# Performance work log

Measured on AMD Instinct MI355X. Metric: run time of the kernel, lower is better.

## Reference

```python
import jax, jax.numpy as jnp
import numpy as np

BS, T, N, M, P = 1024, 128, 128, 256, 256


def _lstm_cell(xin, h, c, Wih, Whh, bih, bhh):
    # PyTorch LSTMCell: gates ordered i, f, g, o
    z = xin @ Wih.T + bih + h @ Whh.T + bhh
    i, f, g, o = jnp.split(z, 4, axis=1)
    i = jax.nn.sigmoid(i); f = jax.nn.sigmoid(f)
    g = jnp.tanh(g); o = jax.nn.sigmoid(o)
    c2 = f * c + i * g
    return o * jnp.tanh(c2), c2


def setup_inputs() -> dict:
    key = jax.random.key(0)
    ks = jax.random.split(key, 24)
    s = 0.05
    return {
        "x": jax.random.normal(ks[0], (BS, T, N), jnp.float32),
        "y_known": jax.random.normal(ks[1], (BS, T, 1), jnp.float32),
        "We": jax.random.normal(ks[2], (T, 2 * M), jnp.float32) * s,
        "Ue": jax.random.normal(ks[3], (T, T), jnp.float32) * s,
        "Ve": jax.random.normal(ks[4], (1, T), jnp.float32) * s,
        "Wih_e": jax.random.normal(ks[5], (4 * M, N), jnp.float32) * s,
        "Whh_e": jax.random.normal(ks[6], (4 * M, M), jnp.float32) * s,
        "bih_e": jax.random.normal(ks[7], (4 * M,), jnp.float32) * s,
        "bhh_e": jax.random.normal(ks[8], (4 * M,), jnp.float32) * s,
        "Wd": jax.random.normal(ks[9], (M, 2 * P), jnp.float32) * s,
        "Ud": jax.random.normal(ks[10], (M, M), jnp.float32) * s,
        "Vd": jax.random.normal(ks[11], (1, M), jnp.float32) * s,
        "Wih_d": jax.random.normal(ks[12], (4 * P, 1), jnp.float32) * s,
        "Whh_d": jax.random.normal(ks[13], (4 * P, P), jnp.float32) * s,
        "bih_d": jax.random.normal(ks[14], (4 * P,), jnp.float32) * s,
        "bhh_d": jax.random.normal(ks[15], (4 * P,), jnp.float32) * s,
        "Wt": jax.random.normal(ks[16], (1, M + 1), jnp.float32) * s,
        "bt": jax.random.normal(ks[17], (1,), jnp.float32) * s,
        "W1": jax.random.normal(ks[18], (P, P + M), jnp.float32) * s,
        "b1": jax.random.normal(ks[19], (P,), jnp.float32) * s,
        "W2": jax.random.normal(ks[20], (1, P), jnp.float32) * s,
        "b2": jax.random.normal(ks[21], (1,), jnp.float32) * s,
    }


def reference(x, y_known, We, Ue, Ve, Wih_e, Whh_e, bih_e, bhh_e,
              Wd, Ud, Vd, Wih_d, Whh_d, bih_d, bhh_d,
              Wt, bt, W1, b1, W2, b2):
    bs, Tl, n = x.shape
    m = Whh_e.shape[1]
    p = Whh_d.shape[1]

    # ---- encoder (input attention) ----
    # U_e(x.permute(0,2,1)): loop-invariant, hoisted. (bs, n, T)
    Ux = jnp.einsum('btn,st->bns', x, Ue)

    def enc_step(carry, _):
        h, s = carry
        hs = jnp.concatenate([h, s], axis=1)            # (bs, 2m)
        ohs = hs @ We.T                                  # (bs, T)
        tanh_sum = jnp.tanh(ohs[:, None, :] + Ux)        # (bs, n, T)
        e = jnp.einsum('bnt,t->bn', tanh_sum, Ve[0])     # (bs, n)
        alpha = jax.nn.softmax(e, axis=1)
        xt = alpha * e                                   # faithful quirk: alpha * e_t
        h2, s2 = _lstm_cell(xt, h, s, Wih_e, Whh_e, bih_e, bhh_e)
        return (h2, s2), h2

    z = jnp.zeros((bs, m), x.dtype)
    _, h_all = jax.lax.scan(enc_step, (z, z), None, length=Tl)
    x1 = jnp.transpose(h_all, (1, 2, 0))                 # (bs, m, T)

    # ---- decoder (temporal attention) ----
    Udx = jnp.einsum('bmt,km->btk', x1, Ud)              # (bs, T, m)

    def dec_step(carry, yt):
        d, s, _ = carry
        ds = jnp.concatenate([d, s], axis=1)             # (bs, 2p)
        ods = ds @ Wd.T                                   # (bs, m)
        tanh_sum = jnp.tanh(ods[:, None, :] + Udx)        # (bs, T, m)
        l = jnp.einsum('btm,m->bt', tanh_sum, Vd[0])      # (bs, T)
        beta = jax.nn.softmax(l, axis=1)
        c = jnp.einsum('bt,bmt->bm', beta, x1)            # (bs, m)
        y_tilde = jnp.concatenate([yt, c], axis=1) @ Wt.T + bt  # (bs, 1)
        d2, s2 = _lstm_cell(y_tilde, d, s, Wih_d, Whh_d, bih_d, bhh_d)
        return (d2, s2, c), None

    zp = jnp.zeros((bs, p), x.dtype)
    zc = jnp.zeros((bs, m), x.dtype)
    (d, _, c), _ = jax.lax.scan(dec_step, (zp, zp, zc),
                                jnp.transpose(y_known, (1, 0, 2)))
    out1 = jnp.concatenate([d, c], axis=1) @ W1.T + b1
    return out1 @ W2.T + b2
```

## Files before the change

kernel.cpp:

```cpp
#include <hip/hip_runtime.h>


typedef unsigned int   uint;
typedef unsigned short ushort;
typedef _Float16 h2v __attribute__((ext_vector_type(2)));

#define O_WEH     0u
#define O_WENCH   32768u
#define O_WDH     229376u
#define O_WHHDH   294912u
#define O_UDT     425984u
#define O_UET     491520u
#define O_W1T     507904u
#define O_BENC    638976u
#define O_BDEC    640000u
#define W_FLOATS  641024u
#define O_X1H     641024u
#define O_BUF     17418240u
#define WS_FLOATS 34195456u

#define C2E 2.8853900817779268f
#define L2E 1.4426950408889634f

#define FMA4(acc, s, w) \
  acc.x = fmaf((s), (w).x, acc.x); \
  acc.y = fmaf((s), (w).y, acc.y); \
  acc.z = fmaf((s), (w).z, acc.z); \
  acc.w = fmaf((s), (w).w, acc.w);

union H2U { uint u; h2v h; _Float16 hs[2]; };

__device__ __forceinline__ float fdot2u(uint w, uint s, float acc) {
  H2U a; a.u = w; H2U b; b.u = s;
  return __builtin_amdgcn_fdot2(a.h, b.h, acc, false);
}
__device__ __forceinline__ uint pk2(float lo, float hi) {
  H2U v; v.hs[0] = (_Float16)lo; v.hs[1] = (_Float16)hi; return v.u;
}
__device__ __forceinline__ float h2lo(uint u) { H2U v; v.u = u; return (float)v.hs[0]; }
__device__ __forceinline__ float h2hi(uint u) { H2U v; v.u = u; return (float)v.hs[1]; }

__device__ __forceinline__ float fsig(float x) {
  return __builtin_amdgcn_rcpf(1.f + __builtin_amdgcn_exp2f(-L2E * x));
}
__device__ __forceinline__ float fth(float x) {
  float r = __builtin_amdgcn_rcpf(1.f + __builtin_amdgcn_exp2f(C2E * x));
  return fmaf(-2.f, r, 1.f);
}

__device__ __forceinline__ float grp4_sum(float v, float* red) {
  #pragma unroll
  for (int o = 32; o > 0; o >>= 1) v += __shfl_xor(v, o);
  __syncthreads();
  int w = threadIdx.x >> 6;
  if ((threadIdx.x & 63) == 0) red[w] = v;
  __syncthreads();
  int wb = w & 4;
  return (red[wb] + red[wb + 1]) + (red[wb + 2] + red[wb + 3]);
}
__device__ __forceinline__ float grp4_max(float v, float* red) {
  #pragma unroll
  for (int o = 32; o > 0; o >>= 1) v = fmaxf(v, __shfl_xor(v, o));
  __syncthreads();
  int w = threadIdx.x >> 6;
  if ((threadIdx.x & 63) == 0) red[w] = v;
  __syncthreads();
  int wb = w & 4;
  return fmaxf(fmaxf(red[wb], red[wb + 1]), fmaxf(red[wb + 2], red[wb + 3]));
}

__global__ __launch_bounds__(256) void prep_k(
    const float* __restrict__ We,    const float* __restrict__ Wih_e,
    const float* __restrict__ Whh_e, const float* __restrict__ Wd,
    const float* __restrict__ Whh_d, const float* __restrict__ W1,
    const float* __restrict__ Ud,    const float* __restrict__ Ue,
    const float* __restrict__ bih_e, const float* __restrict__ bhh_e,
    const float* __restrict__ bih_d, const float* __restrict__ bhh_d,
    float* __restrict__ ws)
{
  uint* wsu = (uint*)ws;
  unsigned idx = blockIdx.x * 256u + threadIdx.x;
  if (idx >= W_FLOATS) return;
  if (idx < 32768u) {
    unsigned kp = idx >> 7, j = idx & 127u;
    wsu[O_WEH + idx] = pk2(We[j * 512u + 2u*kp], We[j * 512u + 2u*kp + 1u]);
  } else if (idx < 229376u) {
    unsigned rel = idx - 32768u;
    unsigned kp = rel >> 10, j = rel & 1023u;
    float v0, v1;
    if (kp < 64u) { v0 = Wih_e[j * 128u + 2u*kp];          v1 = Wih_e[j * 128u + 2u*kp + 1u]; }
    else { unsigned k0 = 2u*(kp - 64u); v0 = Whh_e[j * 256u + k0]; v1 = Whh_e[j * 256u + k0 + 1u]; }
    wsu[O_WENCH + rel] = pk2(v0, v1);
  } else if (idx < 294912u) {
    unsigned rel = idx - 229376u;
    unsigned kp = rel >> 8, kk = rel & 255u;
    wsu[O_WDH + rel] = pk2(Wd[kk * 512u + 2u*kp], Wd[kk * 512u + 2u*kp + 1u]);
  } else if (idx < 425984u) {
    unsigned rel = idx - 294912u;
    unsigned kp = rel >> 10, j = rel & 1023u;
    wsu[O_WHHDH + rel] = pk2(Whh_d[j * 256u + 2u*kp], Whh_d[j * 256u + 2u*kp + 1u]);
  } else if (idx < 491520u) {
    unsigned rel = idx - 425984u;
    unsigned m = rel >> 8, k = rel & 255u;
    ws[O_UDT + rel] = Ud[k * 256u + m];
  } else if (idx < 507904u) {
    unsigned rel = idx - 491520u;
    unsigned t = rel >> 7, s = rel & 127u;
    ws[O_UET + rel] = Ue[s * 128u + t];
  } else if (idx < 638976u) {
    unsigned rel = idx - 507904u;
    unsigned k = rel >> 8, q = rel & 255u;
    ws[O_W1T + rel] = W1[q * 512u + k];
  } else if (idx < 640000u) {
    unsigned rel = idx - 638976u;
    ws[O_BENC + rel] = bih_e[rel] + bhh_e[rel];
  } else {
    unsigned rel = idx - 640000u;
    ws[O_BDEC + rel] = bih_d[rel] + bhh_d[rel];
  }
}

__global__ __launch_bounds__(256) void ux_k(
    const float* __restrict__ x, const float* __restrict__ UeT,
    uint* __restrict__ UxU)
{
  __shared__ float xs[128][32];
  const int b  = blockIdx.x >> 2;
  const int i0 = (blockIdx.x & 3) * 32;
  const int tid = threadIdx.x;
  for (int idx = tid; idx < 4096; idx += 256) {
    int t = idx >> 5, il = idx & 31;
    xs[t][il] = x[(size_t)b * 16384 + t * 128 + i0 + il];
  }
  __syncthreads();
  const int sl = tid & 31;
  const int ig = tid >> 5;
  const float4* UeT4 = (const float4*)UeT;
  float4 acc[4];
  #pragma unroll
  for (int ii = 0; ii < 4; ++ii) acc[ii] = make_float4(0.f, 0.f, 0.f, 0.f);
  for (int t = 0; t < 128; ++t) {
    float4 w = UeT4[t * 32 + sl];
    #pragma unroll
    for (int ii = 0; ii < 4; ++ii) {
      float a = xs[t][ig + 8 * ii];
      FMA4(acc[ii], a, w);
    }
  }
  uint2* U2 = (uint2*)UxU;
  #pragma unroll
  for (int ii = 0; ii < 4; ++ii) {
    int i_loc = i0 + ig + 8 * ii;
    uint2 pk;
    pk.x = pk2(acc[ii].x, acc[ii].y);
    pk.y = pk2(acc[ii].z, acc[ii].w);
    U2[((size_t)b * 128 + i_loc) * 32 + sl] = pk;
  }
}

__global__ __launch_bounds__(256) void udx_k(
    const uint* __restrict__ x1hU, const float* __restrict__ UdT,
    uint* __restrict__ UdxU)
{
  __shared__ float xs[32][256];
  const int b  = blockIdx.x >> 2;
  const int t0 = (blockIdx.x & 3) * 32;
  const int tid = threadIdx.x;
  const uint4* x14 = (const uint4*)x1hU + (size_t)b * 4096;
  for (int it = 0; it < 4; ++it) {
    int f = tid + it * 256;
    int tl = f >> 5, mq = f & 31;
    uint4 u = x14[(size_t)(t0 + tl) * 32 + mq];
    float* d = &xs[tl][mq * 8];
    d[0] = h2lo(u.x); d[1] = h2hi(u.x); d[2] = h2lo(u.y); d[3] = h2hi(u.y);
    d[4] = h2lo(u.z); d[5] = h2hi(u.z); d[6] = h2lo(u.w); d[7] = h2hi(u.w);
  }
  __syncthreads();
  const int kl = tid & 63;
  const int tg = tid >> 6;
  const float4* UdT4 = (const float4*)UdT;
  float4 acc[8];
  #pragma unroll
  for (int tt = 0; tt < 8; ++tt) acc[tt] = make_float4(0.f, 0.f, 0.f, 0.f);
  for (int m = 0; m < 256; ++m) {
    float4 w = UdT4[m * 64 + kl];
    #pragma unroll
    for (int tt = 0; tt < 8; ++tt) {
      float a = xs[tg + 4 * tt][m];
      FMA4(acc[tt], a, w);
    }
  }
  uint2* U2 = (uint2*)UdxU;
  #pragma unroll
  for (int tt = 0; tt < 8; ++tt) {
    uint2 pk;
    pk.x = pk2(acc[tt].x, acc[tt].y);
    pk.y = pk2(acc[tt].z, acc[tt].w);
    U2[((size_t)b * 128 + t0 + tg + 4 * tt) * 64 + kl] = pk;
  }
}

__global__ __launch_bounds__(512, 4) void encoder_k(
    const uint* __restrict__ WeH, const uint* __restrict__ WencH,
    const float* __restrict__ benc, const float* __restrict__ Ve,
    const uint* __restrict__ UxH, uint* __restrict__ x1hU)
{
  __shared__ uint stH[2][256];
  __shared__ uint xtH[2][64];
  __shared__ __align__(16) float part[4096];
  __shared__ float ohs2[2][128];
  __shared__ float xtT[128][2];
  __shared__ float bencS[1024];
  __shared__ float VeS[128];
  __shared__ float red[8];

  const int tid = threadIdx.x;
  const int b0 = blockIdx.x * 2;

  ((uint*)stH)[tid] = 0u;
  for (int i = tid; i < 1024; i += 512) bencS[i] = benc[i];
  if (tid < 128) VeS[tid] = Ve[tid];
  __syncthreads();

  float SVe = 0.f;
  #pragma unroll 8
  for (int s = 0; s < 128; ++s) SVe += VeS[s];

  const uint4* WeH4   = (const uint4*)WeH;
  const uint4* WencH4 = (const uint4*)WencH;
  float4* part4 = (float4*)part;

  const int rB = tid >> 8, iB = (tid >> 1) & 127, sh = tid & 1;
  const uint4* ux4 = (const uint4*)UxH + ((size_t)(b0 + rB) * 128 + iB) * 16 + sh * 8;

  float c_reg = 0.f;

  for (int step = 0; step < 128; ++step) {
    {
      const int j4 = tid & 31, ks = tid >> 5;
      float a0=0,a1=0,a2=0,a3=0,b0=0,b1=0,b2=0,b3=0;
      const int kb = ks * 16;
      #pragma unroll 4
      for (int kp = kb; kp < kb + 16; ++kp) {
        uint4 w = WeH4[kp * 32 + j4];
        uint s0 = stH[0][kp], s1 = stH[1][kp];
        a0 = fdot2u(w.x, s0, a0); a1 = fdot2u(w.y, s0, a1);
        a2 = fdot2u(w.z, s0, a2); a3 = fdot2u(w.w, s0, a3);
        b0 = fdot2u(w.x, s1, b0); b1 = fdot2u(w.y, s1, b1);
        b2 = fdot2u(w.z, s1, b2); b3 = fdot2u(w.w, s1, b3);
      }
      part4[(ks * 2 + 0) * 32 + j4] = make_float4(a0, a1, a2, a3);
      part4[(ks * 2 + 1) * 32 + j4] = make_float4(b0, b1, b2, b3);
    }
    __syncthreads();
    if (tid < 256) {
      const int r = tid >> 7, j = tid & 127;
      float acc = 0.f;
      #pragma unroll
      for (int ks = 0; ks < 16; ++ks) acc += part[(ks * 2 + r) * 128 + j];
      ohs2[r][j] = acc * C2E;
    }
    __syncthreads();
    float e_val;
    {
      float a0 = 0.f, a1 = 0.f, a2 = 0.f, a3 = 0.f;
      const float* oh = ohs2[rB];
      #pragma unroll 2
      for (int so = 0; so < 8; ++so) {
        uint4 u = ux4[so];
        const int s = sh * 64 + so * 8;
        a0 = fmaf(VeS[s+0], __builtin_amdgcn_rcpf(1.f + __builtin_amdgcn_exp2f(fmaf(C2E, h2lo(u.x), oh[s+0]))), a0);
        a1 = fmaf(VeS[s+1], __builtin_amdgcn_rcpf(1.f + __builtin_amdgcn_exp2f(fmaf(C2E, h2hi(u.x), oh[s+1]))), a1);
        a2 = fmaf(VeS[s+2], __builtin_amdgcn_rcpf(1.f + __builtin_amdgcn_exp2f(fmaf(C2E, h2lo(u.y), oh[s+2]))), a2);
        a3 = fmaf(VeS[s+3], __builtin_amdgcn_rcpf(1.f + __builtin_amdgcn_exp2f(fmaf(C2E, h2hi(u.y), oh[s+3]))), a3);
        a0 = fmaf(VeS[s+4], __builtin_amdgcn_rcpf(1.f + __builtin_amdgcn_exp2f(fmaf(C2E, h2lo(u.z), oh[s+4]))), a0);
        a1 = fmaf(VeS[s+5], __builtin_amdgcn_rcpf(1.f + __builtin_amdgcn_exp2f(fmaf(C2E, h2hi(u.z), oh[s+5]))), a1);
        a2 = fmaf(VeS[s+6], __builtin_amdgcn_rcpf(1.f + __builtin_amdgcn_exp2f(fmaf(C2E, h2lo(u.w), oh[s+6]))), a2);
        a3 = fmaf(VeS[s+7], __builtin_amdgcn_rcpf(1.f + __builtin_amdgcn_exp2f(fmaf(C2E, h2hi(u.w), oh[s+7]))), a3);
      }
      float r4 = (a0 + a1) + (a2 + a3);
      r4 += __shfl_xor(r4, 1);
      e_val = fmaf(-2.f, r4, SVe);
    }
    float mx = grp4_max(e_val, red);
    float p  = __builtin_amdgcn_exp2f(L2E * (e_val - mx));
    float sm = grp4_sum(sh == 0 ? p : 0.f, red);
    if (sh == 0) xtT[iB][rB] = p * __builtin_amdgcn_rcpf(sm) * e_val;
    __syncthreads();
    if (tid < 128) {
      const int r = tid >> 6, ii = tid & 63;
      xtH[r][ii] = pk2(xtT[2 * ii][r], xtT[2 * ii + 1][r]);
    }
    __syncthreads();
    {
      const int j4 = tid & 255, ks = tid >> 8;
      float a0=0,a1=0,a2=0,a3=0,b0=0,b1=0,b2=0,b3=0;
      if (ks == 0) {
        #pragma unroll 2
        for (int kp = 0; kp < 64; ++kp) {
          uint4 w = WencH4[kp * 256 + j4];
          uint s0 = xtH[0][kp], s1 = xtH[1][kp];
          a0 = fdot2u(w.x, s0, a0); a1 = fdot2u(w.y, s0, a1);
          a2 = fdot2u(w.z, s0, a2); a3 = fdot2u(w.w, s0, a3);
          b0 = fdot2u(w.x, s1, b0); b1 = fdot2u(w.y, s1, b1);
          b2 = fdot2u(w.z, s1, b2); b3 = fdot2u(w.w, s1, b3);
        }
        #pragma unroll 2
        for (int kp = 64; kp < 96; ++kp) {
          uint4 w = WencH4[kp * 256 + j4];
          uint s0 = stH[0][kp - 64], s1 = stH[1][kp - 64];
          a0 = fdot2u(w.x, s0, a0); a1 = fdot2u(w.y, s0, a1);
          a2 = fdot2u(w.z, s0, a2); a3 = fdot2u(w.w, s0, a3);
          b0 = fdot2u(w.x, s1, b0); b1 = fdot2u(w.y, s1, b1);
          b2 = fdot2u(w.z, s1, b2); b3 = fdot2u(w.w, s1, b3);
        }
      } else {
        #pragma unroll 2
        for (int kp = 96; kp < 192; ++kp) {
          uint4 w = WencH4[kp * 256 + j4];
          uint s0 = stH[0][kp - 64], s1 = stH[1][kp - 64];
          a0 = fdot2u(w.x, s0, a0); a1 = fdot2u(w.y, s0, a1);
          a2 = fdot2u(w.z, s0, a2); a3 = fdot2u(w.w, s0, a3);
          b0 = fdot2u(w.x, s1, b0); b1 = fdot2u(w.y, s1, b1);
          b2 = fdot2u(w.z, s1, b2); b3 = fdot2u(w.w, s1, b3);
        }
      }
      part4[(ks * 2 + 0) * 256 + j4] = make_float4(a0, a1, a2, a3);
      part4[(ks * 2 + 1) * 256 + j4] = make_float4(b0, b1, b2, b3);
    }
    __syncthreads();
    {
      const int r = tid >> 8, j = tid & 255;
      float z0 = bencS[j]       + part[r * 1024 + j]       + part[(2 + r) * 1024 + j];
      float z1 = bencS[256 + j] + part[r * 1024 + 256 + j] + part[(2 + r) * 1024 + 256 + j];
      float z2 = bencS[512 + j] + part[r * 1024 + 512 + j] + part[(2 + r) * 1024 + 512 + j];
      float z3 = bencS[768 + j] + part[r * 1024 + 768 + j] + part[(2 + r) * 1024 + 768 + j];
      float gi = fsig(z0), gf = fsig(z1), gg = fth(z2), go = fsig(z3);
      float c2 = fmaf(gf, c_reg, gi * gg);
      c_reg = c2;
      float h2 = go * fth(c2);
      float hn = __shfl_down(h2, 1);
      float cn = __shfl_down(c2, 1);
      if (!(j & 1)) {
        uint hp = pk2(h2, hn), cp = pk2(c2, cn);
        stH[r][j >> 1] = hp;
        stH[r][128 + (j >> 1)] = cp;
        x1hU[((size_t)(b0 + r) * 128 + step) * 128 + (j >> 1)] = hp;
      }
    }
    __syncthreads();
  }
}

__global__ __launch_bounds__(512, 4) void decoder_k(
    const uint* __restrict__ WdH, const uint* __restrict__ WhhdH,
    const float* __restrict__ W1T, const float* __restrict__ bdec,
    const float* __restrict__ Vd,  const float* __restrict__ WihD,
    const float* __restrict__ Wt,  const float* __restrict__ btp,
    const float* __restrict__ b1,  const float* __restrict__ W2,
    const float* __restrict__ b2p, const float* __restrict__ yk,
    const uint* __restrict__ UdxH, const uint* __restrict__ x1hU,
    float* __restrict__ out)
{
  __shared__ uint stH[2][256];
  __shared__ __align__(16) float part[4096];
  __shared__ float ods2[2][256];
  __shared__ float cT[256][2];
  __shared__ float betaT[128][2];
  __shared__ float wihdS[1024];
  __shared__ float bdecS[1024];
  __shared__ float VdS[256];
  __shared__ float yts[2];
  __shared__ float red[8];

  const int tid = threadIdx.x;
  const int b0 = blockIdx.x * 2;

  ((uint*)stH)[tid] = 0u;
  for (int i = tid; i < 1024; i += 512) { wihdS[i] = WihD[i]; bdecS[i] = bdec[i]; }
  if (tid < 256) VdS[tid] = Vd[tid];
  __syncthreads();

  float SVd = 0.f;
  #pragma unroll 8
  for (int k = 0; k < 256; ++k) SVd += VdS[k];

  const float bt0 = btp[0];
  const uint4*  WdH4   = (const uint4*)WdH;
  const uint4*  WhhdH4 = (const uint4*)WhhdH;
  const float4* W1T4   = (const float4*)W1T;
  float4* part4 = (float4*)part;

  const int rB = tid >> 8, tB = (tid >> 1) & 127, kh = tid & 1;
  const uint4* ud4 = (const uint4*)UdxH + ((size_t)(b0 + rB) * 128 + tB) * 32 + kh * 16;
  const int m8 = tid & 31, rb2 = (tid >> 5) & 1, ts = tid >> 6;
  const uint4* x14 = (const uint4*)x1hU + (size_t)(b0 + rb2) * 4096 + m8;

  float c_reg = 0.f;

  for (int step = 0; step < 128; ++step) {
    {
      const int j4 = tid & 63, ks = tid >> 6;
      float a0=0,a1=0,a2=0,a3=0,b0=0,b1=0,b2=0,b3=0;
      const int kb = ks * 32;
      #pragma unroll 4
      for (int kp = kb; kp < kb + 32; ++kp) {
        uint4 w = WdH4[kp * 64 + j4];
        uint s0 = stH[0][kp], s1 = stH[1][kp];
        a0 = fdot2u(w.x, s0, a0); a1 = fdot2u(w.y, s0, a1);
        a2 = fdot2u(w.z, s0, a2); a3 = fdot2u(w.w, s0, a3);
        b0 = fdot2u(w.x, s1, b0); b1 = fdot2u(w.y, s1, b1);
        b2 = fdot2u(w.z, s1, b2); b3 = fdot2u(w.w, s1, b3);
      }
      part4[(ks * 2 + 0) * 64 + j4] = make_float4(a0, a1, a2, a3);
      part4[(ks * 2 + 1) * 64 + j4] = make_float4(b0, b1, b2, b3);
    }
    __syncthreads();
    {
      const int r = tid >> 8, kk = tid & 255;
      float acc = 0.f;
      #pragma unroll
      for (int ks = 0; ks < 8; ++ks) acc += part[(ks * 2 + r) * 256 + kk];
      ods2[r][kk] = acc * C2E;
    }
    __syncthreads();
    float l_val;
    {
      float a0 = 0.f, a1 = 0.f, a2 = 0.f, a3 = 0.f;
      const float* od = ods2[rB];
      #pragma unroll 2
      for (int ko = 0; ko < 16; ++ko) {
        uint4 u = ud4[ko];
        const int k = kh * 128 + ko * 8;
        a0 = fmaf(VdS[k+0], __builtin_amdgcn_rcpf(1.f + __builtin_amdgcn_exp2f(fmaf(C2E, h2lo(u.x), od[k+0]))), a0);
        a1 = fmaf(VdS[k+1], __builtin_amdgcn_rcpf(1.f + __builtin_amdgcn_exp2f(fmaf(C2E, h2hi(u.x), od[k+1]))), a1);
        a2 = fmaf(VdS[k+2], __builtin_amdgcn_rcpf(1.f + __builtin_amdgcn_exp2f(fmaf(C2E, h2lo(u.y), od[k+2]))), a2);
        a3 = fmaf(VdS[k+3], __builtin_amdgcn_rcpf(1.f + __builtin_amdgcn_exp2f(fmaf(C2E, h2hi(u.y), od[k+3]))), a3);
        a0 = fmaf(VdS[k+4], __builtin_amdgcn_rcpf(1.f + __builtin_amdgcn_exp2f(fmaf(C2E, h2lo(u.z), od[k+4]))), a0);
        a1 = fmaf(VdS[k+5], __builtin_amdgcn_rcpf(1.f + __builtin_amdgcn_exp2f(fmaf(C2E, h2hi(u.z), od[k+5]))), a1);
        a2 = fmaf(VdS[k+6], __builtin_amdgcn_rcpf(1.f + __builtin_amdgcn_exp2f(fmaf(C2E, h2lo(u.w), od[k+6]))), a2);
        a3 = fmaf(VdS[k+7], __builtin_amdgcn_rcpf(1.f + __builtin_amdgcn_exp2f(fmaf(C2E, h2hi(u.w), od[k+7]))), a3);
      }
      float r4 = (a0 + a1) + (a2 + a3);
      r4 += __shfl_xor(r4, 1);
      l_val = fmaf(-2.f, r4, SVd);
    }
    float mx = grp4_max(l_val, red);
    float p  = __builtin_amdgcn_exp2f(L2E * (l_val - mx));
    float sm = grp4_sum(kh == 0 ? p : 0.f, red);
    if (kh == 0) betaT[tB][rB] = p * __builtin_amdgcn_rcpf(sm);
    __syncthreads();
    {
      float c[8];
      #pragma unroll
      for (int e = 0; e < 8; ++e) c[e] = 0.f;
      #pragma unroll 4
      for (int tt = 0; tt < 16; ++tt) {
        const int t = ts * 16 + tt;
        float bv = betaT[t][rb2];
        uint4 u = x14[(size_t)t * 32];
        c[0] = fmaf(bv, h2lo(u.x), c[0]); c[1] = fmaf(bv, h2hi(u.x), c[1]);
        c[2] = fmaf(bv, h2lo(u.y), c[2]); c[3] = fmaf(bv, h2hi(u.y), c[3]);
        c[4] = fmaf(bv, h2lo(u.z), c[4]); c[5] = fmaf(bv, h2hi(u.z), c[5]);
        c[6] = fmaf(bv, h2lo(u.w), c[6]); c[7] = fmaf(bv, h2hi(u.w), c[7]);
      }
      part4[(ts * 2 + rb2) * 64 + m8 * 2]     = make_float4(c[0], c[1], c[2], c[3]);
      part4[(ts * 2 + rb2) * 64 + m8 * 2 + 1] = make_float4(c[4], c[5], c[6], c[7]);
    }
    __syncthreads();
    {
      const int r = tid >> 8, m = tid & 255;
      float v = 0.f;
      #pragma unroll
      for (int t8 = 0; t8 < 8; ++t8) v += part[(t8 * 2 + r) * 256 + m];
      cT[m][r] = v;
    }
    __syncthreads();
    {
      const int r = tid >> 8, i = tid & 255;
      float pv = cT[i][r] * Wt[1 + i];
      float sum = grp4_sum(pv, red);
      if ((tid & 255) == 0) {
        yts[r] = sum + yk[(size_t)(b0 + r) * 128 + step] * Wt[0] + bt0;
      }
    }
    {
      const int j4 = tid & 255, ks = tid >> 8;
      float a0=0,a1=0,a2=0,a3=0,b0=0,b1=0,b2=0,b3=0;
      const int kb = ks * 64;
      #pragma unroll 2
      for (int kp = kb; kp < kb + 64; ++kp) {
        uint4 w = WhhdH4[kp * 256 + j4];
        uint s0 = stH[0][kp], s1 = stH[1][kp];
        a0 = fdot2u(w.x, s0, a0); a1 = fdot2u(w.y, s0, a1);
        a2 = fdot2u(w.z, s0, a2); a3 = fdot2u(w.w, s0, a3);
        b0 = fdot2u(w.x, s1, b0); b1 = fdot2u(w.y, s1, b1);
        b2 = fdot2u(w.z, s1, b2); b3 = fdot2u(w.w, s1, b3);
      }
      part4[(ks * 2 + 0) * 256 + j4] = make_float4(a0, a1, a2, a3);
      part4[(ks * 2 + 1) * 256 + j4] = make_float4(b0, b1, b2, b3);
    }
    __syncthreads();
    {
      const int r = tid >> 8, j = tid & 255;
      float yt = yts[r];
      float z0 = fmaf(yt, wihdS[j],       bdecS[j])       + part[r * 1024 + j]       + part[(2 + r) * 1024 + j];
      float z1 = fmaf(yt, wihdS[256 + j], bdecS[256 + j]) + part[r * 1024 + 256 + j] + part[(2 + r) * 1024 + 256 + j];
      float z2 = fmaf(yt, wihdS[512 + j], bdecS[512 + j]) + part[r * 1024 + 512 + j] + part[(2 + r) * 1024 + 512 + j];
      float z3 = fmaf(yt, wihdS[768 + j], bdecS[768 + j]) + part[r * 1024 + 768 + j] + part[(2 + r) * 1024 + 768 + j];
      float gi = fsig(z0), gf = fsig(z1), gg = fth(z2), go = fsig(z3);
      float c2 = fmaf(gf, c_reg, gi * gg);
      c_reg = c2;
      float d2 = go * fth(c2);
      float dn = __shfl_down(d2, 1);
      float cn = __shfl_down(c2, 1);
      if (!(j & 1)) {
        stH[r][j >> 1] = pk2(d2, dn);
        stH[r][128 + (j >> 1)] = pk2(c2, cn);
      }
    }
    __syncthreads();
  }
  {
    const int l = tid & 63, ks = tid >> 6;
    float a0=0,a1=0,a2=0,a3=0,b0=0,b1=0,b2=0,b3=0;
    const int kb = ks * 64;
    if (ks < 4) {
      for (int k = kb; k < kb + 64; ++k) {
        float4 w = W1T4[k * 64 + l];
        uint u0 = stH[0][k >> 1], u1 = stH[1][k >> 1];
        float d0 = (k & 1) ? h2hi(u0) : h2lo(u0);
        float d1 = (k & 1) ? h2hi(u1) : h2lo(u1);
        a0=fmaf(d0,w.x,a0); a1=fmaf(d0,w.y,a1); a2=fmaf(d0,w.z,a2); a3=fmaf(d0,w.w,a3);
        b0=fmaf(d1,w.x,b0); b1=fmaf(d1,w.y,b1); b2=fmaf(d1,w.z,b2); b3=fmaf(d1,w.w,b3);
      }
    } else {
      for (int k = kb; k < kb + 64; ++k) {
        float4 w = W1T4[k * 64 + l];
        float c0 = cT[k - 256][0], c1 = cT[k - 256][1];
        a0=fmaf(c0,w.x,a0); a1=fmaf(c0,w.y,a1); a2=fmaf(c0,w.z,a2); a3=fmaf(c0,w.w,a3);
        b0=fmaf(c1,w.x,b0); b1=fmaf(c1,w.y,b1); b2=fmaf(c1,w.z,b2); b3=fmaf(c1,w.w,b3);
      }
    }
    part4[(ks * 2 + 0) * 64 + l] = make_float4(a0, a1, a2, a3);
    part4[(ks * 2 + 1) * 64 + l] = make_float4(b0, b1, b2, b3);
  }
  __syncthreads();
  {
    const int r = tid >> 8, q = tid & 255;
    float o1 = b1[q];
    #pragma unroll
    for (int ks = 0; ks < 8; ++ks) o1 += part[(ks * 2 + r) * 256 + q];
    float pv = o1 * W2[q];
    float sum = grp4_sum(pv, red);
    if ((tid & 255) == 0) out[b0 + r] = sum + b2p[0];
  }
}

extern "C" void kernel_launch(void* const* d_in, const int* in_sizes, int n_in,
                              void* d_out, int out_size, void* d_ws, size_t ws_size,
                              hipStream_t stream)
{
  const float* x       = (const float*)d_in[0];
  const float* y_known = (const float*)d_in[1];
  const float* We      = (const float*)d_in[2];
  const float* Ue      = (const float*)d_in[3];
  const float* Ve      = (const float*)d_in[4];
  const float* Wih_e   = (const float*)d_in[5];
  const float* Whh_e   = (const float*)d_in[6];
  const float* bih_e   = (const float*)d_in[7];
  const float* bhh_e   = (const float*)d_in[8];
  const float* Wd      = (const float*)d_in[9];
  const float* Ud      = (const float*)d_in[10];
  const float* Vd      = (const float*)d_in[11];
  const float* Wih_d   = (const float*)d_in[12];
  const float* Whh_d   = (const float*)d_in[13];
  const float* bih_d   = (const float*)d_in[14];
  const float* bhh_d   = (const float*)d_in[15];
  const float* Wt      = (const float*)d_in[16];
  const float* bt      = (const float*)d_in[17];
  const float* W1      = (const float*)d_in[18];
  const float* b1      = (const float*)d_in[19];
  const float* W2      = (const float*)d_in[20];
  const float* b2      = (const float*)d_in[21];

  float* ws  = (float*)d_ws;
  float* out = (float*)d_out;
  if (ws_size < (size_t)WS_FLOATS * 4u) return;

  uint* wsu  = (uint*)ws;
  uint* x1hU = (uint*)(ws + O_X1H);
  uint* bufU = (uint*)(ws + O_BUF);

  prep_k<<<(W_FLOATS + 255) / 256, 256, 0, stream>>>(
      We, Wih_e, Whh_e, Wd, Whh_d, W1, Ud, Ue,
      bih_e, bhh_e, bih_d, bhh_d, ws);

  ux_k<<<4096, 256, 0, stream>>>(x, ws + O_UET, bufU);
  encoder_k<<<512, 512, 0, stream>>>(wsu + O_WEH, wsu + O_WENCH,
                                     ws + O_BENC, Ve, bufU, x1hU);
  udx_k<<<4096, 256, 0, stream>>>(x1hU, ws + O_UDT, bufU);
  decoder_k<<<512, 512, 0, stream>>>(wsu + O_WDH, wsu + O_WHHDH,
                                     ws + O_W1T, ws + O_BDEC, Vd, Wih_d,
                                     Wt, bt, b1, W2, b2, y_known,
                                     bufU, x1hU, out);
}
```

Measured before the change: 7.281 ms.

## Drop softmax max pass, cache attention rows in registers, fuse reductions

The encoder and decoder attention softmax no longer subtracts a block-wide maximum. That removes one full block reduction and two barriers per step, and relies on the scores staying bounded because they are sums of Ve/Vd times tanh. The per-row Ux and Udx half-precision vectors are loaded into registers once before the time loop instead of being re-read from global memory every step. The xt packing now uses a lane shuffle instead of a shared transpose and an extra barrier. The y_tilde and final-output reductions are folded into the preceding stage, and the c/beta shared arrays change layout. The extra 32–64 registers per thread could raise register pressure or cause spills under the launch bounds.

```diff
diff --git a/kernel.cpp b/kernel.cpp
--- a/kernel.cpp
+++ b/kernel.cpp
@@ -48,26 +48,14 @@
   return fmaf(-2.f, r, 1.f);
 }
 
-__device__ __forceinline__ float grp4_sum(float v, float* red) {
-  #pragma unroll
-  for (int o = 32; o > 0; o >>= 1) v += __shfl_xor(v, o);
-  __syncthreads();
-  int w = threadIdx.x >> 6;
-  if ((threadIdx.x & 63) == 0) red[w] = v;
-  __syncthreads();
-  int wb = w & 4;
-  return (red[wb] + red[wb + 1]) + (red[wb + 2] + red[wb + 3]);
-}
-__device__ __forceinline__ float grp4_max(float v, float* red) {
-  #pragma unroll
-  for (int o = 32; o > 0; o >>= 1) v = fmaxf(v, __shfl_xor(v, o));
-  __syncthreads();
-  int w = threadIdx.x >> 6;
-  if ((threadIdx.x & 63) == 0) red[w] = v;
-  __syncthreads();
-  int wb = w & 4;
-  return fmaxf(fmaxf(red[wb], red[wb + 1]), fmaxf(red[wb + 2], red[wb + 3]));
-}
+#define DOT8(w, s0, s1) { \
+  a0 = fdot2u(w.x, s0, a0); a1 = fdot2u(w.y, s0, a1); \
+  a2 = fdot2u(w.z, s0, a2); a3 = fdot2u(w.w, s0, a3); \
+  b0 = fdot2u(w.x, s1, b0); b1 = fdot2u(w.y, s1, b1); \
+  b2 = fdot2u(w.z, s1, b2); b3 = fdot2u(w.w, s1, b3); }
+
+#define ATT_TERM(vv, uu, oo) \
+  fmaf((vv), __builtin_amdgcn_rcpf(1.f + __builtin_amdgcn_exp2f(fmaf(C2E, (uu), (oo)))), 0.f)
 
 __global__ __launch_bounds__(256) void prep_k(
     const float* __restrict__ We,    const float* __restrict__ Wih_e,
@@ -209,7 +197,6 @@
   __shared__ uint xtH[2][64];
   __shared__ __align__(16) float part[4096];
   __shared__ float ohs2[2][128];
-  __shared__ float xtT[128][2];
   __shared__ float bencS[1024];
   __shared__ float VeS[128];
   __shared__ float red[8];
@@ -223,8 +210,7 @@
   __syncthreads();
 
   float SVe = 0.f;
-  #pragma unroll 8
-  for (int s = 0; s < 128; ++s) SVe += VeS[s];
+  for (int s = 0; s < 128; ++s) SVe += Ve[s];
 
   const uint4* WeH4   = (const uint4*)WeH;
   const uint4* WencH4 = (const uint4*)WencH;
@@ -232,6 +218,10 @@
 
   const int rB = tid >> 8, iB = (tid >> 1) & 127, sh = tid & 1;
   const uint4* ux4 = (const uint4*)UxH + ((size_t)(b0 + rB) * 128 + iB) * 16 + sh * 8;
+
+  uint4 uxr[8];
+  #pragma unroll
+  for (int i = 0; i < 8; ++i) uxr[i] = ux4[i];
 
   float c_reg = 0.f;
 
@@ -244,10 +234,7 @@
       for (int kp = kb; kp < kb + 16; ++kp) {
         uint4 w = WeH4[kp * 32 + j4];
         uint s0 = stH[0][kp], s1 = stH[1][kp];
-        a0 = fdot2u(w.x, s0, a0); a1 = fdot2u(w.y, s0, a1);
-        a2 = fdot2u(w.z, s0, a2); a3 = fdot2u(w.w, s0, a3);
-        b0 = fdot2u(w.x, s1, b0); b1 = fdot2u(w.y, s1, b1);
-        b2 = fdot2u(w.z, s1, b2); b3 = fdot2u(w.w, s1, b3);
+        DOT8(w, s0, s1);
       }
       part4[(ks * 2 + 0) * 32 + j4] = make_float4(a0, a1, a2, a3);
       part4[(ks * 2 + 1) * 32 + j4] = make_float4(b0, b1, b2, b3);
@@ -265,31 +252,35 @@
     {
       float a0 = 0.f, a1 = 0.f, a2 = 0.f, a3 = 0.f;
       const float* oh = ohs2[rB];
-      #pragma unroll 2
+      #pragma unroll
       for (int so = 0; so < 8; ++so) {
-        uint4 u = ux4[so];
+        uint4 u = uxr[so];
         const int s = sh * 64 + so * 8;
-        a0 = fmaf(VeS[s+0], __builtin_amdgcn_rcpf(1.f + __builtin_amdgcn_exp2f(fmaf(C2E, h2lo(u.x), oh[s+0]))), a0);
-        a1 = fmaf(VeS[s+1], __builtin_amdgcn_rcpf(1.f + __builtin_amdgcn_exp2f(fmaf(C2E, h2hi(u.x), oh[s+1]))), a1);
-        a2 = fmaf(VeS[s+2], __builtin_amdgcn_rcpf(1.f + __builtin_amdgcn_exp2f(fmaf(C2E, h2lo(u.y), oh[s+2]))), a2);
-        a3 = fmaf(VeS[s+3], __builtin_amdgcn_rcpf(1.f + __builtin_amdgcn_exp2f(fmaf(C2E, h2hi(u.y), oh[s+3]))), a3);
-        a0 = fmaf(VeS[s+4], __builtin_amdgcn_rcpf(1.f + __builtin_amdgcn_exp2f(fmaf(C2E, h2lo(u.z), oh[s+4]))), a0);
-        a1 = fmaf(VeS[s+5], __builtin_amdgcn_rcpf(1.f + __builtin_amdgcn_exp2f(fmaf(C2E, h2hi(u.z), oh[s+5]))), a1);
-        a2 = fmaf(VeS[s+6], __builtin_amdgcn_rcpf(1.f + __builtin_amdgcn_exp2f(fmaf(C2E, h2lo(u.w), oh[s+6]))), a2);
-        a3 = fmaf(VeS[s+7], __builtin_amdgcn_rcpf(1.f + __builtin_amdgcn_exp2f(fmaf(C2E, h2hi(u.w), oh[s+7]))), a3);
+        a0 += ATT_TERM(VeS[s+0], h2lo(u.x), oh[s+0]);
+        a1 += ATT_TERM(VeS[s+1], h2hi(u.x), oh[s+1]);
+        a2 += ATT_TERM(VeS[s+2], h2lo(u.y), oh[s+2]);
+        a3 += ATT_TERM(VeS[s+3], h2hi(u.y), oh[s+3]);
+        a0 += ATT_TERM(VeS[s+4], h2lo(u.z), oh[s+4]);
+        a1 += ATT_TERM(VeS[s+5], h2hi(u.z), oh[s+5]);
+        a2 += ATT_TERM(VeS[s+6], h2lo(u.w), oh[s+6]);
+        a3 += ATT_TERM(VeS[s+7], h2hi(u.w), oh[s+7]);
       }
       float r4 = (a0 + a1) + (a2 + a3);
       r4 += __shfl_xor(r4, 1);
       e_val = fmaf(-2.f, r4, SVe);
     }
-    float mx = grp4_max(e_val, red);
-    float p  = __builtin_amdgcn_exp2f(L2E * (e_val - mx));
-    float sm = grp4_sum(sh == 0 ? p : 0.f, red);
-    if (sh == 0) xtT[iB][rB] = p * __builtin_amdgcn_rcpf(sm) * e_val;
-    __syncthreads();
-    if (tid < 128) {
-      const int r = tid >> 6, ii = tid & 63;
-      xtH[r][ii] = pk2(xtT[2 * ii][r], xtT[2 * ii + 1][r]);
+    {
+      float p  = __builtin_amdgcn_exp2f(L2E * e_val);
+      float ps = (sh == 0) ? p : 0.f;
+      #pragma unroll
+      for (int o = 1; o < 64; o <<= 1) ps += __shfl_xor(ps, o);
+      if ((tid & 63) == 0) red[tid >> 6] = ps;
+      __syncthreads();
+      const int base = (tid >> 6) & 4;
+      float sm = (red[base+0] + red[base+1]) + (red[base+2] + red[base+3]);
+      float xt = p * __builtin_amdgcn_rcpf(sm) * e_val;
+      float xn = __shfl_down(xt, 2);
+      if ((tid & 3) == 0) xtH[rB][iB >> 1] = pk2(xt, xn);
     }
     __syncthreads();
     {
@@ -300,29 +291,20 @@
         for (int kp = 0; kp < 64; ++kp) {
           uint4 w = WencH4[kp * 256 + j4];
           uint s0 = xtH[0][kp], s1 = xtH[1][kp];
-          a0 = fdot2u(w.x, s0, a0); a1 = fdot2u(w.y, s0, a1);
-          a2 = fdot2u(w.z, s0, a2); a3 = fdot2u(w.w, s0, a3);
-          b0 = fdot2u(w.x, s1, b0); b1 = fdot2u(w.y, s1, b1);
-          b2 = fdot2u(w.z, s1, b2); b3 = fdot2u(w.w, s1, b3);
+          DOT8(w, s0, s1);
         }
         #pragma unroll 2
         for (int kp = 64; kp < 96; ++kp) {
           uint4 w = WencH4[kp * 256 + j4];
           uint s0 = stH[0][kp - 64], s1 = stH[1][kp - 64];
-          a0 = fdot2u(w.x, s0, a0); a1 = fdot2u(w.y, s0, a1);
-          a2 = fdot2u(w.z, s0, a2); a3 = fdot2u(w.w, s0, a3);
-          b0 = fdot2u(w.x, s1, b0); b1 = fdot2u(w.y, s1, b1);
-          b2 = fdot2u(w.z, s1, b2); b3 = fdot2u(w.w, s1, b3);
+          DOT8(w, s0, s1);
         }
       } else {
         #pragma unroll 2
         for (int kp = 96; kp < 192; ++kp) {
           uint4 w = WencH4[kp * 256 + j4];
           uint s0 = stH[0][kp - 64], s1 = stH[1][kp - 64];
-          a0 = fdot2u(w.x, s0, a0); a1 = fdot2u(w.y, s0, a1);
-          a2 = fdot2u(w.z, s0, a2); a3 = fdot2u(w.w, s0, a3);
-          b0 = fdot2u(w.x, s1, b0); b1 = fdot2u(w.y, s1, b1);
-          b2 = fdot2u(w.z, s1, b2); b3 = fdot2u(w.w, s1, b3);
+          DOT8(w, s0, s1);
         }
       }
       part4[(ks * 2 + 0) * 256 + j4] = make_float4(a0, a1, a2, a3);
@@ -365,8 +347,8 @@
   __shared__ uint stH[2][256];
   __shared__ __align__(16) float part[4096];
   __shared__ float ods2[2][256];
-  __shared__ float cT[256][2];
-  __shared__ float betaT[128][2];
+  __shared__ float cT[2][256];
+  __shared__ float betaS[2][128];
   __shared__ float wihdS[1024];
   __shared__ float bdecS[1024];
   __shared__ float VdS[256];
@@ -382,10 +364,9 @@
   __syncthreads();
 
   float SVd = 0.f;
-  #pragma unroll 8
-  for (int k = 0; k < 256; ++k) SVd += VdS[k];
-
-  const float bt0 = btp[0];
+  for (int k = 0; k < 256; ++k) SVd += Vd[k];
+
+  const float bt0 = btp[0], Wt0 = Wt[0];
   const uint4*  WdH4   = (const uint4*)WdH;
   const uint4*  WhhdH4 = (const uint4*)WhhdH;
   const float4* W1T4   = (const float4*)W1T;
@@ -394,7 +375,11 @@
   const int rB = tid >> 8, tB = (tid >> 1) & 127, kh = tid & 1;
   const uint4* ud4 = (const uint4*)UdxH + ((size_t)(b0 + rB) * 128 + tB) * 32 + kh * 16;
   const int m8 = tid & 31, rb2 = (tid >> 5) & 1, ts = tid >> 6;
-  const uint4* x14 = (const uint4*)x1hU + (size_t)(b0 + rb2) * 4096 + m8;
+  const uint2* x12 = (const uint2*)x1hU + (size_t)(b0 + rb2) * 8192;
+
+  uint4 udr[16];
+  #pragma unroll
+  for (int i = 0; i < 16; ++i) udr[i] = ud4[i];
 
   float c_reg = 0.f;
 
@@ -407,10 +392,7 @@
       for (int kp = kb; kp < kb + 32; ++kp) {
         uint4 w = WdH4[kp * 64 + j4];
         uint s0 = stH[0][kp], s1 = stH[1][kp];
-        a0 = fdot2u(w.x, s0, a0); a1 = fdot2u(w.y, s0, a1);
-        a2 = fdot2u(w.z, s0, a2); a3 = fdot2u(w.w, s0, a3);
-        b0 = fdot2u(w.x, s1, b0); b1 = fdot2u(w.y, s1, b1);
-        b2 = fdot2u(w.z, s1, b2); b3 = fdot2u(w.w, s1, b3);
+        DOT8(w, s0, s1);
       }
       part4[(ks * 2 + 0) * 64 + j4] = make_float4(a0, a1, a2, a3);
       part4[(ks * 2 + 1) * 64 + j4] = make_float4(b0, b1, b2, b3);
@@ -428,44 +410,52 @@
     {
       float a0 = 0.f, a1 = 0.f, a2 = 0.f, a3 = 0.f;
       const float* od = ods2[rB];
-      #pragma unroll 2
+      #pragma unroll
       for (int ko = 0; ko < 16; ++ko) {
-        uint4 u = ud4[ko];
+        uint4 u = udr[ko];
         const int k = kh * 128 + ko * 8;
-        a0 = fmaf(VdS[k+0], __builtin_amdgcn_rcpf(1.f + __builtin_amdgcn_exp2f(fmaf(C2E, h2lo(u.x), od[k+0]))), a0);
-        a1 = fmaf(VdS[k+1], __builtin_amdgcn_rcpf(1.f + __builtin_amdgcn_exp2f(fmaf(C2E, h2hi(u.x), od[k+1]))), a1);
-        a2 = fmaf(VdS[k+2], __builtin_amdgcn_rcpf(1.f + __builtin_amdgcn_exp2f(fmaf(C2E, h2lo(u.y), od[k+2]))), a2);
-        a3 = fmaf(VdS[k+3], __builtin_amdgcn_rcpf(1.f + __builtin_amdgcn_exp2f(fmaf(C2E, h2hi(u.y), od[k+3]))), a3);
-        a0 = fmaf(VdS[k+4], __builtin_amdgcn_rcpf(1.f + __builtin_amdgcn_exp2f(fmaf(C2E, h2lo(u.z), od[k+4]))), a0);
-        a1 = fmaf(VdS[k+5], __builtin_amdgcn_rcpf(1.f + __builtin_amdgcn_exp2f(fmaf(C2E, h2hi(u.z), od[k+5]))), a1);
-        a2 = fmaf(VdS[k+6], __builtin_amdgcn_rcpf(1.f + __builtin_amdgcn_exp2f(fmaf(C2E, h2lo(u.w), od[k+6]))), a2);
-        a3 = fmaf(VdS[k+7], __builtin_amdgcn_rcpf(1.f + __builtin_amdgcn_exp2f(fmaf(C2E, h2hi(u.w), od[k+7]))), a3);
+        a0 += ATT_TERM(VdS[k+0], h2lo(u.x), od[k+0]);
+        a1 += ATT_TERM(VdS[k+1], h2hi(u.x), od[k+1]);
+        a2 += ATT_TERM(VdS[k+2], h2lo(u.y), od[k+2]);
+        a3 += ATT_TERM(VdS[k+3], h2hi(u.y), od[k+3]);
+        a0 += ATT_TERM(VdS[k+4], h2lo(u.z), od[k+4]);
+        a1 += ATT_TERM(VdS[k+5], h2hi(u.z), od[k+5]);
+        a2 += ATT_TERM(VdS[k+6], h2lo(u.w), od[k+6]);
+        a3 += ATT_TERM(VdS[k+7], h2hi(u.w), od[k+7]);
       }
       float r4 = (a0 + a1) + (a2 + a3);
       r4 += __shfl_xor(r4, 1);
       l_val = fmaf(-2.f, r4, SVd);
     }
-    float mx = grp4_max(l_val, red);
-    float p  = __builtin_amdgcn_exp2f(L2E * (l_val - mx));
-    float sm = grp4_sum(kh == 0 ? p : 0.f, red);
-    if (kh == 0) betaT[tB][rB] = p * __builtin_amdgcn_rcpf(sm);
-    __syncthreads();
-    {
-      float c[8];
-      #pragma unroll
-      for (int e = 0; e < 8; ++e) c[e] = 0.f;
+    {
+      float p  = __builtin_amdgcn_exp2f(L2E * l_val);
+      float ps = (kh == 0) ? p : 0.f;
+      #pragma unroll
+      for (int o = 1; o < 64; o <<= 1) ps += __shfl_xor(ps, o);
+      if ((tid & 63) == 0) red[tid >> 6] = ps;
+      __syncthreads();
+      const int base = (tid >> 6) & 4;
+      float sm = (red[base+0] + red[base+1]) + (red[base+2] + red[base+3]);
+      if (kh == 0) betaS[rB][tB] = p * __builtin_amdgcn_rcpf(sm);
+    }
+    __syncthreads();
+    {
+      float c0=0,c1=0,c2=0,c3=0,c4=0,c5=0,c6=0,c7=0;
+      const float* bS = betaS[rb2];
+      const uint2* xr = x12 + m8;
       #pragma unroll 4
       for (int tt = 0; tt < 16; ++tt) {
         const int t = ts * 16 + tt;
-        float bv = betaT[t][rb2];
-        uint4 u = x14[(size_t)t * 32];
-        c[0] = fmaf(bv, h2lo(u.x), c[0]); c[1] = fmaf(bv, h2hi(u.x), c[1]);
-        c[2] = fmaf(bv, h2lo(u.y), c[2]); c[3] = fmaf(bv, h2hi(u.y), c[3]);
-        c[4] = fmaf(bv, h2lo(u.z), c[4]); c[5] = fmaf(bv, h2hi(u.z), c[5]);
-        c[6] = fmaf(bv, h2lo(u.w), c[6]); c[7] = fmaf(bv, h2hi(u.w), c[7]);
-      }
-      part4[(ts * 2 + rb2) * 64 + m8 * 2]     = make_float4(c[0], c[1], c[2], c[3]);
-      part4[(ts * 2 + rb2) * 64 + m8 * 2 + 1] = make_float4(c[4], c[5], c[6], c[7]);
+        float bv = bS[t];
+        uint2 u  = xr[t * 64];
+        uint2 u2 = xr[t * 64 + 32];
+        c0 = fmaf(bv, h2lo(u.x),  c0); c1 = fmaf(bv, h2hi(u.x),  c1);
+        c2 = fmaf(bv, h2lo(u.y),  c2); c3 = fmaf(bv, h2hi(u.y),  c3);
+        c4 = fmaf(bv, h2lo(u2.x), c4); c5 = fmaf(bv, h2hi(u2.x), c5);
+        c6 = fmaf(bv, h2lo(u2.y), c6); c7 = fmaf(bv, h2hi(u2.y), c7);
+      }
+      part4[(ts * 2 + rb2) * 64 + m8]      = make_float4(c0, c1, c2, c3);
+      part4[(ts * 2 + rb2) * 64 + 32 + m8] = make_float4(c4, c5, c6, c7);
     }
     __syncthreads();
     {
@@ -473,15 +463,16 @@
       float v = 0.f;
       #pragma unroll
       for (int t8 = 0; t8 < 8; ++t8) v += part[(t8 * 2 + r) * 256 + m];
-      cT[m][r] = v;
-    }
-    __syncthreads();
-    {
-      const int r = tid >> 8, i = tid & 255;
-      float pv = cT[i][r] * Wt[1 + i];
-      float sum = grp4_sum(pv, red);
+      cT[r][m] = v;
+      float pv = v * Wt[1 + m];
+      #pragma unroll
+      for (int o = 1; o < 64; o <<= 1) pv += __shfl_xor(pv, o);
+      if ((tid & 63) == 0) red[tid >> 6] = pv;
+      __syncthreads();
       if ((tid & 255) == 0) {
-        yts[r] = sum + yk[(size_t)(b0 + r) * 128 + step] * Wt[0] + bt0;
+        const int base = r * 4;
+        float s = (red[base] + red[base+1]) + (red[base+2] + red[base+3]);
+        yts[r] = s + yk[(size_t)(b0 + r) * 128 + step] * Wt0 + bt0;
       }
     }
     {
@@ -492,10 +483,7 @@
       for (int kp = kb; kp < kb + 64; ++kp) {
         uint4 w = WhhdH4[kp * 256 + j4];
         uint s0 = stH[0][kp], s1 = stH[1][kp];
-        a0 = fdot2u(w.x, s0, a0); a1 = fdot2u(w.y, s0, a1);
-        a2 = fdot2u(w.z, s0, a2); a3 = fdot2u(w.w, s0, a3);
-        b0 = fdot2u(w.x, s1, b0); b1 = fdot2u(w.y, s1, b1);
-        b2 = fdot2u(w.z, s1, b2); b3 = fdot2u(w.w, s1, b3);
+        DOT8(w, s0, s1);
       }
       part4[(ks * 2 + 0) * 256 + j4] = make_float4(a0, a1, a2, a3);
       part4[(ks * 2 + 1) * 256 + j4] = make_float4(b0, b1, b2, b3);
@@ -515,8 +503,8 @@
       float dn = __shfl_down(d2, 1);
       float cn = __shfl_down(c2, 1);
       if (!(j & 1)) {
-        stH[r][j >> 1] = pk2(d2, dn);
-        stH[r][128 + (j >> 1)] = pk2(c2, cn);
+        stH[rB][j >> 1] = pk2(d2, dn);
+        stH[rB][128 + (j >> 1)] = pk2(c2, cn);
       }
     }
     __syncthreads();
@@ -537,7 +525,7 @@
     } else {
       for (int k = kb; k < kb + 64; ++k) {
         float4 w = W1T4[k * 64 + l];
-        float c0 = cT[k - 256][0], c1 = cT[k - 256][1];
+        float c0 = cT[0][k - 256], c1 = cT[1][k - 256];
         a0=fmaf(c0,w.x,a0); a1=fmaf(c0,w.y,a1); a2=fmaf(c0,w.z,a2); a3=fmaf(c0,w.w,a3);
         b0=fmaf(c1,w.x,b0); b1=fmaf(c1,w.y,b1); b2=fmaf(c1,w.z,b2); b3=fmaf(c1,w.w,b3);
       }
@@ -552,8 +540,15 @@
     #pragma unroll
     for (int ks = 0; ks < 8; ++ks) o1 += part[(ks * 2 + r) * 256 + q];
     float pv = o1 * W2[q];
-    float sum = grp4_sum(pv, red);
-    if ((tid & 255) == 0) out[b0 + r] = sum + b2p[0];
+    #pragma unroll
+    for (int o = 1; o < 64; o <<= 1) pv += __shfl_xor(pv, o);
+    if ((tid & 63) == 0) red[tid >> 6] = pv;
+    __syncthreads();
+    if ((tid & 255) == 0) {
+      const int base = r * 4;
+      float s = (red[base] + red[base+1]) + (red[base+2] + red[base+3]);
+      out[b0 + r] = s + b2p[0];
+    }
   }
 }
 
```

Result: slower. 11.03 ms (+51.4%).
